# Performance work log

Measured on AMD Instinct MI355X. Metric: run time of the kernel, lower is better.

## Reference

```python
import jax, jax.numpy as jnp
import numpy as np

N = 100000
E = 1600000
NFEAT, NHID, NCLASS = 500, 128, 40


def setup_inputs() -> dict:
    key = jax.random.key(0)
    ks = jax.random.split(key, 12)
    x = jax.random.normal(ks[0], (N, NFEAT), dtype=jnp.float32)
    row = jax.random.randint(ks[1], (E,), 0, N, dtype=jnp.int32)
    col = jax.random.randint(ks[2], (E,), 0, N, dtype=jnp.int32)
    # precomputed normalized adjacency values (D^-1/2 A D^-1/2 style)
    edge_weight = jax.random.uniform(ks[3], (E,), dtype=jnp.float32) / 16.0
    def lin(k, fi, fo):
        s = 1.0 / np.sqrt(fi)
        return jax.random.uniform(k, (fi, fo), dtype=jnp.float32, minval=-s, maxval=s)
    return {
        "x": x, "row": row, "col": col, "edge_weight": edge_weight,
        "W1": lin(ks[4], NFEAT, NHID), "b1": jnp.zeros((NHID,), jnp.float32),
        "W2": lin(ks[5], NHID, NHID), "b2": jnp.zeros((NHID,), jnp.float32),
        "W3": lin(ks[6], NHID, NHID), "b3": jnp.zeros((NHID,), jnp.float32),
        "W4": lin(ks[7], NHID, NCLASS), "b4": jnp.zeros((NCLASS,), jnp.float32),
    }


def gcn_layer(h, row, col, edge_weight, W, b):
    # support = h @ W ; out = spmm(adj, support) + b  (Kipf GraphConvolution)
    support = h @ W                                   # [N, Fout]
    msgs = edge_weight[:, None] * support[col]        # [E, Fout] gather on source nodes
    agg = jax.ops.segment_sum(msgs, row, num_segments=N)  # scatter-add to dest nodes
    return agg + b


def reference(x, row, col, edge_weight, W1, b1, W2, b2, W3, b3, W4, b4):
    # dropout is identity in eval mode (training=False)
    h = jax.nn.relu(gcn_layer(x, row, col, edge_weight, W1, b1))
    h = jax.nn.relu(gcn_layer(h, row, col, edge_weight, W2, b2))
    h = jax.nn.relu(gcn_layer(h, row, col, edge_weight, W3, b3))
    h = gcn_layer(h, row, col, edge_weight, W4, b4)
    return jax.nn.log_softmax(h, axis=1)
```

## Files before the change

### kernel.cpp

```cpp
#include <hip/hip_runtime.h>
#include <cstdint>
#include <cstddef>

#define NFEAT 500
#define NHID  128
#define NCLASS 40

typedef __attribute__((ext_vector_type(8))) short bf16x8;
typedef __attribute__((ext_vector_type(4))) float f32x4;

__device__ __forceinline__ unsigned short f2bf(float f) {
    union { float f; unsigned u; } v; v.f = f;
    unsigned u = v.u;
    unsigned r = u + 0x7FFF + ((u >> 16) & 1);
    return (unsigned short)(r >> 16);
}
__device__ __forceinline__ float bf2f(unsigned short h) {
    union { unsigned u; float f; } v; v.u = ((unsigned)h) << 16; return v.f;
}

__device__ __forceinline__ bf16x8 cvt8(float4 a, float4 b) {
    union { bf16x8 v; unsigned u[4]; } r;
    r.u[0] = (unsigned)f2bf(a.x) | ((unsigned)f2bf(a.y) << 16);
    r.u[1] = (unsigned)f2bf(a.z) | ((unsigned)f2bf(a.w) << 16);
    r.u[2] = (unsigned)f2bf(b.x) | ((unsigned)f2bf(b.y) << 16);
    r.u[3] = (unsigned)f2bf(b.z) | ((unsigned)f2bf(b.w) << 16);
    return r.v;
}


__global__ void k_hist(const int* __restrict__ row, int E, int* __restrict__ counts) {
    int i = blockIdx.x * 256 + threadIdx.x;
    if (i < E) atomicAdd(&counts[row[i]], 1);
}

__global__ void k_block_sum(const int* __restrict__ counts, int n, int* __restrict__ partials) {
    __shared__ int tmp[256];
    int i = blockIdx.x * 256 + threadIdx.x;
    tmp[threadIdx.x] = (i < n) ? counts[i] : 0;
    __syncthreads();
    for (int o = 128; o > 0; o >>= 1) {
        if (threadIdx.x < o) tmp[threadIdx.x] += tmp[threadIdx.x + o];
        __syncthreads();
    }
    if (threadIdx.x == 0) partials[blockIdx.x] = tmp[0];
}

__global__ void k_scan_partials(int* __restrict__ partials, int nb) {
    __shared__ int tmp[512];
    int t = threadIdx.x;
    int v = (t < nb) ? partials[t] : 0;
    tmp[t] = v;
    __syncthreads();
    for (int o = 1; o < 512; o <<= 1) {
        int add = (t >= o) ? tmp[t - o] : 0;
        __syncthreads();
        tmp[t] += add;
        __syncthreads();
    }
    if (t < nb) partials[t] = tmp[t] - v;
}

__global__ void k_scan_counts(int* __restrict__ counts, const int* __restrict__ partials,
                              int* __restrict__ row_ptr, int n) {
    __shared__ int tmp[256];
    int t = threadIdx.x;
    int i = blockIdx.x * 256 + t;
    int v = (i < n) ? counts[i] : 0;
    tmp[t] = v;
    __syncthreads();
    for (int o = 1; o < 256; o <<= 1) {
        int add = (t >= o) ? tmp[t - o] : 0;
        __syncthreads();
        tmp[t] += add;
        __syncthreads();
    }
    int incl = tmp[t];
    int base = partials[blockIdx.x];
    if (i < n) {
        row_ptr[i] = base + incl - v;
        counts[i] = 0;
    }
    if (i == n - 1) row_ptr[n] = base + incl;
}

__global__ void k_scatter(const int* __restrict__ row, const int* __restrict__ col,
                          const float* __restrict__ w, int E,
                          const int* __restrict__ row_ptr, int* __restrict__ cursor,
                          uint2* __restrict__ csr_cw) {
    int i = blockIdx.x * 256 + threadIdx.x;
    if (i < E) {
        int r = row[i];
        int p = row_ptr[r] + atomicAdd(&cursor[r], 1);
        csr_cw[p] = make_uint2((unsigned)col[i], __float_as_uint(w[i]));
    }
}


__global__ void k_prep_w(const float* __restrict__ W, unsigned short* __restrict__ Wt,
                         int K, int Norig, int Nt, int Kpad) {
    int idx = blockIdx.x * 256 + threadIdx.x;
    if (idx >= Nt * Kpad) return;
    int n = idx / Kpad, k = idx % Kpad;
    unsigned short v = 0;
    if (k < K && n < Norig) v = f2bf(W[(size_t)k * Norig + n]);
    Wt[idx] = v;
}


#define LDA1(V0, V1, V2, V3, IT)                                   \
    do {                                                           \
        const float* p0_ = ap0 + (IT) * 32;                        \
        const float* p1_ = ap1 + (IT) * 32;                        \
        V0 = *(const float4*)p0_;  V1 = *(const float4*)(p0_ + 4); \
        V2 = *(const float4*)p1_;  V3 = *(const float4*)(p1_ + 4); \
    } while (0)

#define CMP1(V0, V1, V2, V3, IT)                                                             \
    do {                                                                                     \
        bf16x8 bfr_[8];                                                                      \
        _Pragma("unroll")                                                                    \
        for (int ni_ = 0; ni_ < 8; ni_++)                                                    \
            bfr_[ni_] = *(const bf16x8*)(bp + (size_t)(ni_ * 16) * 512 + (IT) * 32);         \
        bf16x8 af0_ = cvt8(V0, V1);                                                          \
        bf16x8 af1_ = cvt8(V2, V3);                                                          \
        _Pragma("unroll")                                                                    \
        for (int ni_ = 0; ni_ < 8; ni_++) {                                                  \
            acc[0][ni_] = __builtin_amdgcn_mfma_f32_16x16x32_bf16(af0_, bfr_[ni_], acc[0][ni_], 0, 0, 0); \
            acc[1][ni_] = __builtin_amdgcn_mfma_f32_16x16x32_bf16(af1_, bfr_[ni_], acc[1][ni_], 0, 0, 0); \
        }                                                                                    \
    } while (0)

__global__ __launch_bounds__(256) void k_gemm_l1(const float* __restrict__ A,
                                                 const unsigned short* __restrict__ Wt,
                                                 unsigned short* __restrict__ C, int M) {
    constexpr int K = 500;
    const int t = threadIdx.x;
    const int lane = t & 63;
    const int l15 = lane & 15, quad = lane >> 4;
    const int wave = blockIdx.x * 4 + (t >> 6);
    const int m0 = wave * 32;

    const int r0 = m0 + l15, r1 = r0 + 16;
    const int rc0 = (r0 < M) ? r0 : M - 1;
    const int rc1 = (r1 < M) ? r1 : M - 1;
    const float* ap0 = A + (size_t)rc0 * K + quad * 8;
    const float* ap1 = A + (size_t)rc1 * K + quad * 8;
    const unsigned short* bp = Wt + (size_t)l15 * 512 + quad * 8;

    f32x4 acc[2][8];
#pragma unroll
    for (int mi = 0; mi < 2; mi++)
#pragma unroll
        for (int ni = 0; ni < 8; ni++)
            acc[mi][ni] = (f32x4){0.f, 0.f, 0.f, 0.f};

    float4 sa0, sa1, sa2, sa3;
    float4 sb0, sb1, sb2, sb3;
    float4 sc0, sc1, sc2, sc3;

    LDA1(sa0, sa1, sa2, sa3, 0);
    LDA1(sb0, sb1, sb2, sb3, 1);
#pragma unroll
    for (int it = 0; it < 15; it += 3) {
        LDA1(sc0, sc1, sc2, sc3, it + 2);
        CMP1(sa0, sa1, sa2, sa3, it);
        if (it + 3 < 15) LDA1(sa0, sa1, sa2, sa3, it + 3);
        CMP1(sb0, sb1, sb2, sb3, it + 1);
        if (it + 4 < 15) LDA1(sb0, sb1, sb2, sb3, it + 4);
        CMP1(sc0, sc1, sc2, sc3, it + 2);
    }

    {
        float va[8], vb[8];
#pragma unroll
        for (int j = 0; j < 8; j++) {
            int gk = 480 + quad * 8 + j;
            va[j] = (gk < K) ? ap0[15 * 32 + j] : 0.f;
            vb[j] = (gk < K) ? ap1[15 * 32 + j] : 0.f;
        }
        float4 t0 = make_float4(va[0], va[1], va[2], va[3]);
        float4 t1 = make_float4(va[4], va[5], va[6], va[7]);
        float4 t2 = make_float4(vb[0], vb[1], vb[2], vb[3]);
        float4 t3 = make_float4(vb[4], vb[5], vb[6], vb[7]);
        CMP1(t0, t1, t2, t3, 15);
    }

#pragma unroll
    for (int mi = 0; mi < 2; mi++) {
#pragma unroll
        for (int r = 0; r < 4; r++) {
            int gm = m0 + mi * 16 + quad * 4 + r;
#pragma unroll
            for (int ni = 0; ni < 8; ni++)
                C[(size_t)gm * 128 + ni * 16 + l15] = f2bf(acc[mi][ni][r]);
        }
    }
}


template<int TN, int CN, int CPITCH>
__global__ __launch_bounds__(256) void k_gemm_b(const unsigned short* __restrict__ A,
                                                const unsigned short* __restrict__ Wt,
                                                unsigned short* __restrict__ C) {
    const int t = threadIdx.x;
    const int lane = t & 63;
    const int l15 = lane & 15, quad = lane >> 4;
    const int wave = blockIdx.x * 4 + (t >> 6);
    const int m0 = wave * 32;
    const int r0 = m0 + l15, r1 = r0 + 16;

    const unsigned short* ap0 = A + (size_t)r0 * 128 + quad * 8;
    const unsigned short* ap1 = A + (size_t)r1 * 128 + quad * 8;
    const unsigned short* bp = Wt + (size_t)l15 * 128 + quad * 8;

    f32x4 acc[2][TN];
#pragma unroll
    for (int mi = 0; mi < 2; mi++)
#pragma unroll
        for (int ni = 0; ni < TN; ni++)
            acc[mi][ni] = (f32x4){0.f, 0.f, 0.f, 0.f};

    bf16x8 a00 = *(const bf16x8*)(ap0);       bf16x8 a01 = *(const bf16x8*)(ap1);
    bf16x8 a10 = *(const bf16x8*)(ap0 + 32);  bf16x8 a11 = *(const bf16x8*)(ap1 + 32);
    bf16x8 a20 = *(const bf16x8*)(ap0 + 64);  bf16x8 a21 = *(const bf16x8*)(ap1 + 64);
    bf16x8 a30 = *(const bf16x8*)(ap0 + 96);  bf16x8 a31 = *(const bf16x8*)(ap1 + 96);

#define CMPB(AF0, AF1, IT)                                                                   \
    do {                                                                                     \
        bf16x8 bfr_[TN];                                                                     \
        _Pragma("unroll")                                                                    \
        for (int ni_ = 0; ni_ < TN; ni_++)                                                   \
            bfr_[ni_] = *(const bf16x8*)(bp + (size_t)(ni_ * 16) * 128 + (IT) * 32);         \
        _Pragma("unroll")                                                                    \
        for (int ni_ = 0; ni_ < TN; ni_++) {                                                 \
            acc[0][ni_] = __builtin_amdgcn_mfma_f32_16x16x32_bf16(AF0, bfr_[ni_], acc[0][ni_], 0, 0, 0); \
            acc[1][ni_] = __builtin_amdgcn_mfma_f32_16x16x32_bf16(AF1, bfr_[ni_], acc[1][ni_], 0, 0, 0); \
        }                                                                                    \
    } while (0)

    CMPB(a00, a01, 0);
    CMPB(a10, a11, 1);
    CMPB(a20, a21, 2);
    CMPB(a30, a31, 3);
#undef CMPB

#pragma unroll
    for (int mi = 0; mi < 2; mi++) {
#pragma unroll
        for (int r = 0; r < 4; r++) {
            int gm = m0 + mi * 16 + quad * 4 + r;
#pragma unroll
            for (int ni = 0; ni < TN; ni++) {
                int gn = ni * 16 + l15;
                if (gn < CN) C[(size_t)gm * CPITCH + gn] = f2bf(acc[mi][ni][r]);
            }
        }
    }
}


__global__ __launch_bounds__(256) void k_spmm128(const unsigned short* __restrict__ S,
                                                 const int* __restrict__ rp,
                                                 const uint2* __restrict__ cw,
                                                 const float* __restrict__ bias,
                                                 unsigned short* __restrict__ out,
                                                 int n, int do_relu) {
    int wid  = threadIdx.x >> 6;
    int lane = threadIdx.x & 63;
    int node = blockIdx.x * 4 + wid;
    if (node >= n) return;
    int s = rp[node], e = rp[node + 1];
    float a0x = 0.f, a0y = 0.f, a1x = 0.f, a1y = 0.f;
    float a2x = 0.f, a2y = 0.f, a3x = 0.f, a3y = 0.f;
    int i = s;
    for (; i + 4 <= e; i += 4) {
        uint2 e0 = cw[i], e1 = cw[i + 1], e2 = cw[i + 2], e3 = cw[i + 3];
        unsigned v0 = ((const unsigned*)(S + (size_t)e0.x * NHID))[lane];
        unsigned v1 = ((const unsigned*)(S + (size_t)e1.x * NHID))[lane];
        unsigned v2 = ((const unsigned*)(S + (size_t)e2.x * NHID))[lane];
        unsigned v3 = ((const unsigned*)(S + (size_t)e3.x * NHID))[lane];
        float w0 = __uint_as_float(e0.y), w1 = __uint_as_float(e1.y);
        float w2 = __uint_as_float(e2.y), w3 = __uint_as_float(e3.y);
        a0x = fmaf(w0, bf2f((unsigned short)v0), a0x); a0y = fmaf(w0, bf2f((unsigned short)(v0 >> 16)), a0y);
        a1x = fmaf(w1, bf2f((unsigned short)v1), a1x); a1y = fmaf(w1, bf2f((unsigned short)(v1 >> 16)), a1y);
        a2x = fmaf(w2, bf2f((unsigned short)v2), a2x); a2y = fmaf(w2, bf2f((unsigned short)(v2 >> 16)), a2y);
        a3x = fmaf(w3, bf2f((unsigned short)v3), a3x); a3y = fmaf(w3, bf2f((unsigned short)(v3 >> 16)), a3y);
    }
    for (; i < e; i++) {
        uint2 e0 = cw[i];
        unsigned v0 = ((const unsigned*)(S + (size_t)e0.x * NHID))[lane];
        float w0 = __uint_as_float(e0.y);
        a0x = fmaf(w0, bf2f((unsigned short)v0), a0x); a0y = fmaf(w0, bf2f((unsigned short)(v0 >> 16)), a0y);
    }
    float ax = (a0x + a1x) + (a2x + a3x) + bias[lane * 2];
    float ay = (a0y + a1y) + (a2y + a3y) + bias[lane * 2 + 1];
    if (do_relu) {
        ax = fmaxf(ax, 0.f);
        ay = fmaxf(ay, 0.f);
    }
    unsigned o = (unsigned)f2bf(ax) | ((unsigned)f2bf(ay) << 16);
    __builtin_nontemporal_store(o, (unsigned*)(out + (size_t)node * NHID) + lane);
}


__global__ __launch_bounds__(256) void k_spmm40_lsm(const unsigned short* __restrict__ S,
                                                    const int* __restrict__ rp,
                                                    const uint2* __restrict__ cw,
                                                    const float* __restrict__ bias,
                                                    float* __restrict__ out,
                                                    int n) {
    int wid  = threadIdx.x >> 6;
    int lane = threadIdx.x & 63;
    int node = blockIdx.x * 4 + wid;
    if (node >= n) return;
    int s = rp[node], e = rp[node + 1];
    float a0 = 0.f, a1 = 0.f, a2 = 0.f, a3 = 0.f;
    int i = s;
    bool act = lane < NCLASS;
    for (; i + 4 <= e; i += 4) {
        uint2 e0 = cw[i], e1 = cw[i + 1], e2 = cw[i + 2], e3 = cw[i + 3];
        if (act) {
            float v0 = bf2f(S[(size_t)e0.x * NCLASS + lane]);
            float v1 = bf2f(S[(size_t)e1.x * NCLASS + lane]);
            float v2 = bf2f(S[(size_t)e2.x * NCLASS + lane]);
            float v3 = bf2f(S[(size_t)e3.x * NCLASS + lane]);
            a0 = fmaf(__uint_as_float(e0.y), v0, a0);
            a1 = fmaf(__uint_as_float(e1.y), v1, a1);
            a2 = fmaf(__uint_as_float(e2.y), v2, a2);
            a3 = fmaf(__uint_as_float(e3.y), v3, a3);
        }
    }
    for (; i < e; i++) {
        uint2 e0 = cw[i];
        if (act) a0 = fmaf(__uint_as_float(e0.y), bf2f(S[(size_t)e0.x * NCLASS + lane]), a0);
    }
    float acc = (a0 + a1) + (a2 + a3);
    float logit = act ? acc + bias[lane] : -INFINITY;
    float m = logit;
#pragma unroll
    for (int o = 32; o >= 1; o >>= 1) m = fmaxf(m, __shfl_xor(m, o, 64));
    float ex = act ? expf(logit - m) : 0.f;
    float ssum = ex;
#pragma unroll
    for (int o = 32; o >= 1; o >>= 1) ssum += __shfl_xor(ssum, o, 64);
    if (act) {
        float r = logit - m - logf(ssum);
        __builtin_nontemporal_store(r, out + (size_t)node * NCLASS + lane);
    }
}


extern "C" void kernel_launch(void* const* d_in, const int* in_sizes, int n_in,
                              void* d_out, int out_size, void* d_ws, size_t ws_size,
                              hipStream_t stream) {
    const float* x  = (const float*)d_in[0];
    const int* row  = (const int*)d_in[1];
    const int* col  = (const int*)d_in[2];
    const float* ew = (const float*)d_in[3];
    const float* W1 = (const float*)d_in[4];
    const float* b1 = (const float*)d_in[5];
    const float* W2 = (const float*)d_in[6];
    const float* b2 = (const float*)d_in[7];
    const float* W3 = (const float*)d_in[8];
    const float* b3 = (const float*)d_in[9];
    const float* W4 = (const float*)d_in[10];
    const float* b4 = (const float*)d_in[11];
    float* out = (float*)d_out;

    const int Nn = in_sizes[0] / NFEAT;
    const int E  = in_sizes[1];
    const int NB = (Nn + 255) / 256;
    const int Mpad = (Nn + 127) & ~127;

    char* ws = (char*)d_ws;
    size_t off = 0;
    auto alloc = [&](size_t bytes) {
        size_t o = off;
        off = (off + bytes + 255) & ~(size_t)255;
        return o;
    };
    int*   row_ptr  = (int*)(ws + alloc((size_t)(Nn + 1) * 4));
    int*   counts   = (int*)(ws + alloc((size_t)Nn * 4));
    int*   partials = (int*)(ws + alloc((size_t)NB * 4));
    uint2* csr_cw   = (uint2*)(ws + alloc((size_t)E * 8));
    unsigned short* Sb  = (unsigned short*)(ws + alloc((size_t)Mpad * NHID * 2));
    unsigned short* Hb  = (unsigned short*)(ws + alloc((size_t)Mpad * NHID * 2));
    unsigned short* S4b = (unsigned short*)(ws + alloc((size_t)Mpad * NCLASS * 2));
    unsigned short* Wt1 = (unsigned short*)(ws + alloc((size_t)128 * 512 * 2));
    unsigned short* Wt2 = (unsigned short*)(ws + alloc((size_t)128 * 128 * 2));
    unsigned short* Wt3 = (unsigned short*)(ws + alloc((size_t)128 * 128 * 2));
    unsigned short* Wt4 = (unsigned short*)(ws + alloc((size_t)48 * 128 * 2));

    k_prep_w<<<(128 * 512 + 255) / 256, 256, 0, stream>>>(W1, Wt1, NFEAT, NHID, 128, 512);
    k_prep_w<<<(128 * 128 + 255) / 256, 256, 0, stream>>>(W2, Wt2, NHID, NHID, 128, 128);
    k_prep_w<<<(128 * 128 + 255) / 256, 256, 0, stream>>>(W3, Wt3, NHID, NHID, 128, 128);
    k_prep_w<<<(48 * 128 + 255) / 256, 256, 0, stream>>>(W4, Wt4, NHID, NCLASS, 48, 128);

    (void)hipMemsetAsync(counts, 0, (size_t)Nn * 4, stream);
    k_hist<<<(E + 255) / 256, 256, 0, stream>>>(row, E, counts);
    k_block_sum<<<NB, 256, 0, stream>>>(counts, Nn, partials);
    k_scan_partials<<<1, 512, 0, stream>>>(partials, NB);
    k_scan_counts<<<NB, 256, 0, stream>>>(counts, partials, row_ptr, Nn);
    k_scatter<<<(E + 255) / 256, 256, 0, stream>>>(row, col, ew, E, row_ptr, counts, csr_cw);

    const int gblocks = Mpad / 128;
    const int spmm_blocks = (Nn + 3) / 4;

    k_gemm_l1<<<gblocks, 256, 0, stream>>>(x, Wt1, Sb, Nn);
    k_spmm128<<<spmm_blocks, 256, 0, stream>>>(Sb, row_ptr, csr_cw, b1, Hb, Nn, 1);
    k_gemm_b<8, 128, 128><<<gblocks, 256, 0, stream>>>(Hb, Wt2, Sb);
    k_spmm128<<<spmm_blocks, 256, 0, stream>>>(Sb, row_ptr, csr_cw, b2, Hb, Nn, 1);
    k_gemm_b<8, 128, 128><<<gblocks, 256, 0, stream>>>(Hb, Wt3, Sb);
    k_spmm128<<<spmm_blocks, 256, 0, stream>>>(Sb, row_ptr, csr_cw, b3, Hb, Nn, 1);
    k_gemm_b<3, 40, 40><<<gblocks, 256, 0, stream>>>(Hb, Wt4, S4b);
    k_spmm40_lsm<<<spmm_blocks, 256, 0, stream>>>(S4b, row_ptr, csr_cw, b4, out, Nn);
}
```

Before: 893.5 us.

## Stream layer-1 GEMM A tiles via global_load_lds into swizzled triple-buffered LDS

The layer-1 GEMM now loads the fp32 input rows with direct global-to-LDS loads into a per-wave, three-slot LDS ring using an XOR swizzle, instead of register-prefetching float4s. Each wave waits on vmcnt, reads the fragments from LDS, and issues the load three iterations ahead. This is meant to give coalesced 16-byte row-chunk loads and deeper prefetch while cutting register pressure. The cost is 48KB of LDS per block, which may limit occupancy, and the correctness of the manual waitcnt ordering.

```diff
diff --git a/kernel.cpp b/kernel.cpp
--- a/kernel.cpp
+++ b/kernel.cpp
@@ -8,6 +8,8 @@
 
 typedef __attribute__((ext_vector_type(8))) short bf16x8;
 typedef __attribute__((ext_vector_type(4))) float f32x4;
+typedef const __attribute__((address_space(1))) void* gas_t;
+typedef __attribute__((address_space(3))) void* las_t;
 
 __device__ __forceinline__ unsigned short f2bf(float f) {
     union { float f; unsigned u; } v; v.f = f;
@@ -108,45 +110,42 @@
 }
 
 
-#define LDA1(V0, V1, V2, V3, IT)                                   \
-    do {                                                           \
-        const float* p0_ = ap0 + (IT) * 32;                        \
-        const float* p1_ = ap1 + (IT) * 32;                        \
-        V0 = *(const float4*)p0_;  V1 = *(const float4*)(p0_ + 4); \
-        V2 = *(const float4*)p1_;  V3 = *(const float4*)(p1_ + 4); \
-    } while (0)
-
-#define CMP1(V0, V1, V2, V3, IT)                                                             \
-    do {                                                                                     \
-        bf16x8 bfr_[8];                                                                      \
-        _Pragma("unroll")                                                                    \
-        for (int ni_ = 0; ni_ < 8; ni_++)                                                    \
-            bfr_[ni_] = *(const bf16x8*)(bp + (size_t)(ni_ * 16) * 512 + (IT) * 32);         \
-        bf16x8 af0_ = cvt8(V0, V1);                                                          \
-        bf16x8 af1_ = cvt8(V2, V3);                                                          \
-        _Pragma("unroll")                                                                    \
-        for (int ni_ = 0; ni_ < 8; ni_++) {                                                  \
-            acc[0][ni_] = __builtin_amdgcn_mfma_f32_16x16x32_bf16(af0_, bfr_[ni_], acc[0][ni_], 0, 0, 0); \
-            acc[1][ni_] = __builtin_amdgcn_mfma_f32_16x16x32_bf16(af1_, bfr_[ni_], acc[1][ni_], 0, 0, 0); \
-        }                                                                                    \
+#define GLD1(SLOT, IT)                                                            \
+    do {                                                                          \
+        __builtin_amdgcn_global_load_lds((gas_t)(gs0 + (IT) * 32),                \
+            (las_t)(lb + (SLOT) * 1024 + 0 * 256), 16, 0, 0);                     \
+        __builtin_amdgcn_global_load_lds((gas_t)(gs1 + (IT) * 32),                \
+            (las_t)(lb + (SLOT) * 1024 + 1 * 256), 16, 0, 0);                     \
+        __builtin_amdgcn_global_load_lds((gas_t)(gs2 + (IT) * 32),                \
+            (las_t)(lb + (SLOT) * 1024 + 2 * 256), 16, 0, 0);                     \
+        __builtin_amdgcn_global_load_lds((gas_t)(gs3 + (IT) * 32),                \
+            (las_t)(lb + (SLOT) * 1024 + 3 * 256), 16, 0, 0);                     \
     } while (0)
 
 __global__ __launch_bounds__(256) void k_gemm_l1(const float* __restrict__ A,
                                                  const unsigned short* __restrict__ Wt,
                                                  unsigned short* __restrict__ C, int M) {
-    constexpr int K = 500;
+    __shared__ __align__(16) float lds[4][3][1024];
     const int t = threadIdx.x;
     const int lane = t & 63;
+    const int w = t >> 6;
     const int l15 = lane & 15, quad = lane >> 4;
-    const int wave = blockIdx.x * 4 + (t >> 6);
+    const int wave = blockIdx.x * 4 + w;
     const int m0 = wave * 32;
 
-    const int r0 = m0 + l15, r1 = r0 + 16;
-    const int rc0 = (r0 < M) ? r0 : M - 1;
-    const int rc1 = (r1 < M) ? r1 : M - 1;
-    const float* ap0 = A + (size_t)rc0 * K + quad * 8;
-    const float* ap1 = A + (size_t)rc1 * K + quad * 8;
-    const unsigned short* bp = Wt + (size_t)l15 * 512 + quad * 8;
+    const int srow = lane >> 3;
+    const int sch  = (lane & 7) ^ srow;
+    int sr0 = m0 + srow,      sr1 = m0 + 8 + srow;
+    int sr2 = m0 + 16 + srow, sr3 = m0 + 24 + srow;
+    sr0 = (sr0 < M) ? sr0 : M - 1;
+    sr1 = (sr1 < M) ? sr1 : M - 1;
+    sr2 = (sr2 < M) ? sr2 : M - 1;
+    sr3 = (sr3 < M) ? sr3 : M - 1;
+    const float* gs0 = A + (size_t)sr0 * NFEAT + sch * 4;
+    const float* gs1 = A + (size_t)sr1 * NFEAT + sch * 4;
+    const float* gs2 = A + (size_t)sr2 * NFEAT + sch * 4;
+    const float* gs3 = A + (size_t)sr3 * NFEAT + sch * 4;
+    float* lb = &lds[w][0][0];
 
     f32x4 acc[2][8];
 #pragma unroll
@@ -155,35 +154,62 @@
         for (int ni = 0; ni < 8; ni++)
             acc[mi][ni] = (f32x4){0.f, 0.f, 0.f, 0.f};
 
-    float4 sa0, sa1, sa2, sa3;
-    float4 sb0, sb1, sb2, sb3;
-    float4 sc0, sc1, sc2, sc3;
-
-    LDA1(sa0, sa1, sa2, sa3, 0);
-    LDA1(sb0, sb1, sb2, sb3, 1);
-#pragma unroll
-    for (int it = 0; it < 15; it += 3) {
-        LDA1(sc0, sc1, sc2, sc3, it + 2);
-        CMP1(sa0, sa1, sa2, sa3, it);
-        if (it + 3 < 15) LDA1(sa0, sa1, sa2, sa3, it + 3);
-        CMP1(sb0, sb1, sb2, sb3, it + 1);
-        if (it + 4 < 15) LDA1(sb0, sb1, sb2, sb3, it + 4);
-        CMP1(sc0, sc1, sc2, sc3, it + 2);
+    const unsigned short* bp = Wt + (size_t)l15 * 512 + quad * 8;
+    const int s0  = (quad * 2) ^ (l15 & 7);
+    const int ro0 = l15 * 32, ro1 = (16 + l15) * 32;
+
+    GLD1(0, 0);
+    GLD1(1, 1);
+    GLD1(2, 2);
+
+#pragma unroll
+    for (int j = 0; j < 15; ++j) {
+        const int slot = j % 3;
+        asm volatile("s_waitcnt vmcnt(8)" ::: "memory");
+        bf16x8 bfr[8];
+#pragma unroll
+        for (int ni = 0; ni < 8; ni++)
+            bfr[ni] = *(const bf16x8*)(bp + (size_t)(ni * 16) * 512 + j * 32);
+        const float* sb = lb + slot * 1024;
+        float4 x0 = *(const float4*)(sb + ro0 + s0 * 4);
+        float4 x1 = *(const float4*)(sb + ro0 + (s0 ^ 1) * 4);
+        float4 y0 = *(const float4*)(sb + ro1 + s0 * 4);
+        float4 y1 = *(const float4*)(sb + ro1 + (s0 ^ 1) * 4);
+        asm volatile("s_waitcnt lgkmcnt(0)" ::: "memory");
+        if (j + 3 < 15) GLD1(slot, j + 3);
+        bf16x8 af0 = cvt8(x0, x1);
+        bf16x8 af1 = cvt8(y0, y1);
+#pragma unroll
+        for (int ni = 0; ni < 8; ni++) {
+            acc[0][ni] = __builtin_amdgcn_mfma_f32_16x16x32_bf16(af0, bfr[ni], acc[0][ni], 0, 0, 0);
+            acc[1][ni] = __builtin_amdgcn_mfma_f32_16x16x32_bf16(af1, bfr[ni], acc[1][ni], 0, 0, 0);
+        }
     }
 
     {
+        const int r0 = m0 + l15, r1 = r0 + 16;
+        const int rc0 = (r0 < M) ? r0 : M - 1;
+        const int rc1 = (r1 < M) ? r1 : M - 1;
+        const float* ap0 = A + (size_t)rc0 * NFEAT + quad * 8;
+        const float* ap1 = A + (size_t)rc1 * NFEAT + quad * 8;
+        bf16x8 bfr[8];
+#pragma unroll
+        for (int ni = 0; ni < 8; ni++)
+            bfr[ni] = *(const bf16x8*)(bp + (size_t)(ni * 16) * 512 + 15 * 32);
         float va[8], vb[8];
 #pragma unroll
-        for (int j = 0; j < 8; j++) {
-            int gk = 480 + quad * 8 + j;
-            va[j] = (gk < K) ? ap0[15 * 32 + j] : 0.f;
-            vb[j] = (gk < K) ? ap1[15 * 32 + j] : 0.f;
-        }
-        float4 t0 = make_float4(va[0], va[1], va[2], va[3]);
-        float4 t1 = make_float4(va[4], va[5], va[6], va[7]);
-        float4 t2 = make_float4(vb[0], vb[1], vb[2], vb[3]);
-        float4 t3 = make_float4(vb[4], vb[5], vb[6], vb[7]);
-        CMP1(t0, t1, t2, t3, 15);
+        for (int jj = 0; jj < 8; jj++) {
+            int gk = 480 + quad * 8 + jj;
+            va[jj] = (gk < NFEAT) ? ap0[480 + jj] : 0.f;
+            vb[jj] = (gk < NFEAT) ? ap1[480 + jj] : 0.f;
+        }
+        bf16x8 af0 = cvt8(make_float4(va[0], va[1], va[2], va[3]), make_float4(va[4], va[5], va[6], va[7]));
+        bf16x8 af1 = cvt8(make_float4(vb[0], vb[1], vb[2], vb[3]), make_float4(vb[4], vb[5], vb[6], vb[7]));
+#pragma unroll
+        for (int ni = 0; ni < 8; ni++) {
+            acc[0][ni] = __builtin_amdgcn_mfma_f32_16x16x32_bf16(af0, bfr[ni], acc[0][ni], 0, 0, 0);
+            acc[1][ni] = __builtin_amdgcn_mfma_f32_16x16x32_bf16(af1, bfr[ni], acc[1][ni], 0, 0, 0);
+        }
     }
 
 #pragma unroll
```

Measured after the change: 885.0 us. Within noise of the previous version (-0.9%).
